# Performance work log

Measured on AMD Instinct MI355X. Metric: run time of the kernel, lower is better.

## Reference

```python
import jax, jax.numpy as jnp
import numpy as np

N_NODES = 50000
N_EDGES = 600000
D_FEAT = 128
HIDDEN = 128
OUT = 64


def sage_conv(x, src, dst, Wl, bl, Wr, n_nodes):
    # message = x[src] gathered per edge; mean-aggregated at dst
    msg = x[src]                                            # [E, d]
    agg = jax.ops.segment_sum(msg, dst, num_segments=n_nodes)   # [N, d]
    cnt = jax.ops.segment_sum(jnp.ones((src.shape[0],), x.dtype), dst,
                              num_segments=n_nodes)             # [N]
    mean = agg / jnp.maximum(cnt, 1.0)[:, None]
    # PyG SAGEConv: lin_l(mean_neighbors) + lin_r(x_root); only lin_l has bias
    return mean @ Wl + bl + x @ Wr


def setup_inputs() -> dict:
    key = jax.random.key(0)
    ks = jax.random.split(key, 7)
    x = jax.random.normal(ks[0], (N_NODES, D_FEAT), dtype=jnp.float32)
    edge_index = jax.random.randint(ks[1], (2, N_EDGES), 0, N_NODES, dtype=jnp.int64)
    s1 = 1.0 / np.sqrt(D_FEAT)
    s2 = 1.0 / np.sqrt(HIDDEN)
    W1l = jax.random.normal(ks[2], (D_FEAT, HIDDEN), dtype=jnp.float32) * s1
    b1l = jnp.zeros((HIDDEN,), dtype=jnp.float32)
    W1r = jax.random.normal(ks[3], (D_FEAT, HIDDEN), dtype=jnp.float32) * s1
    W2l = jax.random.normal(ks[4], (HIDDEN, OUT), dtype=jnp.float32) * s2
    b2l = jnp.zeros((OUT,), dtype=jnp.float32)
    W2r = jax.random.normal(ks[5], (HIDDEN, OUT), dtype=jnp.float32) * s2
    return {"x": x, "edge_index": edge_index, "W1l": W1l, "b1l": b1l,
            "W1r": W1r, "W2l": W2l, "b2l": b2l, "W2r": W2r}


def reference(x, edge_index, W1l, b1l, W1r, W2l, b2l, W2r):
    n = x.shape[0]
    src, dst = edge_index[0], edge_index[1]
    h = sage_conv(x, src, dst, W1l, b1l, W1r, n)
    h = jax.nn.relu(h)
    out = sage_conv(h, src, dst, W2l, b2l, W2r, n)
    return out
```

## Files before the change

### kernel.cpp

```cpp
#include <hip/hip_runtime.h>
#include <cstdint>
#include <cstddef>

#define D 128
#define O2 64
#define PAD 136
#define CAP 64

typedef __attribute__((ext_vector_type(8))) short bf16x8;
typedef __attribute__((ext_vector_type(4))) float f32x4;

__device__ inline unsigned short f2bf(float f) {
  union { float f; uint32_t u; } v; v.f = f;
  uint32_t r = v.u + 0x7FFF + ((v.u >> 16) & 1);
  return (unsigned short)(r >> 16);
}
__device__ inline float bf_lo(uint32_t w) {
  union { uint32_t u; float f; } v; v.u = w << 16; return v.f;
}
__device__ inline float bf_hi(uint32_t w) {
  union { uint32_t u; float f; } v; v.u = w & 0xFFFF0000u; return v.f;
}

__device__ __forceinline__ void gather16(
    const unsigned short* __restrict__ xb, const unsigned short* __restrict__ bucket,
    int cnt, int j, float a[16])
{
  int p = 0;
  for (; p + 8 <= cnt; p += 8) {
    uint4 bi = *(const uint4*)(bucket + p);
    int s[8];
    s[0] = bi.x & 0xFFFF; s[1] = bi.x >> 16;
    s[2] = bi.y & 0xFFFF; s[3] = bi.y >> 16;
    s[4] = bi.z & 0xFFFF; s[5] = bi.z >> 16;
    s[6] = bi.w & 0xFFFF; s[7] = bi.w >> 16;
    uint4 v0[8], v1[8];
    #pragma unroll
    for (int q = 0; q < 8; q++) {
      const unsigned short* r = xb + (size_t)s[q] * 128 + j * 16;
      v0[q] = *(const uint4*)r;
      v1[q] = *(const uint4*)(r + 8);
    }
    #pragma unroll
    for (int q = 0; q < 8; q++) {
      a[0]+=bf_lo(v0[q].x); a[1]+=bf_hi(v0[q].x);
      a[2]+=bf_lo(v0[q].y); a[3]+=bf_hi(v0[q].y);
      a[4]+=bf_lo(v0[q].z); a[5]+=bf_hi(v0[q].z);
      a[6]+=bf_lo(v0[q].w); a[7]+=bf_hi(v0[q].w);
      a[8]+=bf_lo(v1[q].x); a[9]+=bf_hi(v1[q].x);
      a[10]+=bf_lo(v1[q].y); a[11]+=bf_hi(v1[q].y);
      a[12]+=bf_lo(v1[q].z); a[13]+=bf_hi(v1[q].z);
      a[14]+=bf_lo(v1[q].w); a[15]+=bf_hi(v1[q].w);
    }
  }
  for (; p + 4 <= cnt; p += 4) {
    uint2 bi = *(const uint2*)(bucket + p);
    int s[4];
    s[0] = bi.x & 0xFFFF; s[1] = bi.x >> 16;
    s[2] = bi.y & 0xFFFF; s[3] = bi.y >> 16;
    uint4 v0[4], v1[4];
    #pragma unroll
    for (int q = 0; q < 4; q++) {
      const unsigned short* r = xb + (size_t)s[q] * 128 + j * 16;
      v0[q] = *(const uint4*)r;
      v1[q] = *(const uint4*)(r + 8);
    }
    #pragma unroll
    for (int q = 0; q < 4; q++) {
      a[0]+=bf_lo(v0[q].x); a[1]+=bf_hi(v0[q].x);
      a[2]+=bf_lo(v0[q].y); a[3]+=bf_hi(v0[q].y);
      a[4]+=bf_lo(v0[q].z); a[5]+=bf_hi(v0[q].z);
      a[6]+=bf_lo(v0[q].w); a[7]+=bf_hi(v0[q].w);
      a[8]+=bf_lo(v1[q].x); a[9]+=bf_hi(v1[q].x);
      a[10]+=bf_lo(v1[q].y); a[11]+=bf_hi(v1[q].y);
      a[12]+=bf_lo(v1[q].z); a[13]+=bf_hi(v1[q].z);
      a[14]+=bf_lo(v1[q].w); a[15]+=bf_hi(v1[q].w);
    }
  }
  for (; p < cnt; p++) {
    const unsigned short* rA = xb + (size_t)bucket[p] * 128 + j * 16;
    uint4 vA0 = *(const uint4*)rA, vA1 = *(const uint4*)(rA + 8);
    a[0]+=bf_lo(vA0.x); a[1]+=bf_hi(vA0.x); a[2]+=bf_lo(vA0.y); a[3]+=bf_hi(vA0.y);
    a[4]+=bf_lo(vA0.z); a[5]+=bf_hi(vA0.z); a[6]+=bf_lo(vA0.w); a[7]+=bf_hi(vA0.w);
    a[8]+=bf_lo(vA1.x); a[9]+=bf_hi(vA1.x); a[10]+=bf_lo(vA1.y); a[11]+=bf_hi(vA1.y);
    a[12]+=bf_lo(vA1.z); a[13]+=bf_hi(vA1.z); a[14]+=bf_lo(vA1.w); a[15]+=bf_hi(vA1.w);
  }
}

__global__ __launch_bounds__(256) void prep_all(
    const int* __restrict__ src, const int* __restrict__ dst,
    int* __restrict__ deg, unsigned short* __restrict__ eidx, int n_edges,
    const float* __restrict__ x, const float* __restrict__ W1l,
    const float* __restrict__ W1r, const float* __restrict__ W2l,
    const float* __restrict__ W2r, unsigned short* __restrict__ xb,
    unsigned short* __restrict__ WT1, unsigned short* __restrict__ WT2,
    int n_nodes, int edge_blocks, int xb_blocks)
{
  int b = blockIdx.x;
  if (b < edge_blocks) {
    const int half = n_edges >> 1;
    int e = b * 256 + threadIdx.x;
    if (e < half) {
      int d0 = dst[e],        d1 = dst[e + half];
      int s0 = src[e],        s1 = src[e + half];
      int p0 = atomicAdd(&deg[d0], 1);
      int p1 = atomicAdd(&deg[d1], 1);
      if (p0 < CAP)
        __builtin_nontemporal_store((unsigned short)s0, eidx + (size_t)d0 * CAP + p0);
      if (p1 < CAP)
        __builtin_nontemporal_store((unsigned short)s1, eidx + (size_t)d1 * CAP + p1);
    }
  } else if (b < edge_blocks + xb_blocks) {
    int i = (b - edge_blocks) * 256 + threadIdx.x;
    if (i < n_nodes * 32) {
      int n = i >> 5, q = i & 31;
      float4 v = ((const float4*)x)[(size_t)n * 32 + q];
      unsigned long long o =
          (unsigned long long)f2bf(v.x)
        | ((unsigned long long)f2bf(v.y) << 16)
        | ((unsigned long long)f2bf(v.z) << 32)
        | ((unsigned long long)f2bf(v.w) << 48);
      __builtin_nontemporal_store(o, (unsigned long long*)(xb + (size_t)n * 128 + q * 4));
    }
  } else {
    int t = (b - edge_blocks - xb_blocks) * 256 + threadIdx.x;
    if (t < 128 * 256) {
      int n = t >> 8, k = t & 255;
      float w = (k < 128) ? W1l[(size_t)k * 128 + n] : W1r[(size_t)(k - 128) * 128 + n];
      WT1[t] = f2bf(w);
    } else {
      int u = t - 128 * 256;
      if (u < 128 * 128) {
        int n = u >> 7, k = u & 127;
        float w = (n < 64) ? W2l[(size_t)k * 64 + n] : W2r[(size_t)k * 64 + (n - 64)];
        WT2[u] = f2bf(w);
      }
    }
  }
}

__global__ __launch_bounds__(256, 5) void fused_l12(
    const unsigned short* __restrict__ xb, const unsigned short* __restrict__ eidx,
    const int* __restrict__ deg, const unsigned short* __restrict__ WT1,
    const unsigned short* __restrict__ WT2, const float* __restrict__ b1l,
    unsigned short* __restrict__ hl, float* __restrict__ outp, int n_nodes)
{
  __shared__ unsigned short s_m[32 * PAD];
  __shared__ unsigned short s_h[32 * PAD];
  const int NB0 = blockIdx.x * 32;

  {
    const int j = threadIdx.x & 7;
    const int g = threadIdx.x >> 3;
    const int n = NB0 + g;
    float a[16];
    #pragma unroll
    for (int i = 0; i < 16; i++) a[i] = 0.f;
    float ic = 0.f;
    if (n < n_nodes) {
      const int dg = deg[n];
      const int cnt = min(dg, CAP);
      gather16(xb, eidx + (size_t)n * CAP, cnt, j, a);
      ic = 1.0f / fmaxf((float)dg, 1.0f);
    }
    uint4 o0, o1;
    o0.x = ((uint32_t)f2bf(a[1]*ic) << 16) | f2bf(a[0]*ic);
    o0.y = ((uint32_t)f2bf(a[3]*ic) << 16) | f2bf(a[2]*ic);
    o0.z = ((uint32_t)f2bf(a[5]*ic) << 16) | f2bf(a[4]*ic);
    o0.w = ((uint32_t)f2bf(a[7]*ic) << 16) | f2bf(a[6]*ic);
    o1.x = ((uint32_t)f2bf(a[9]*ic) << 16) | f2bf(a[8]*ic);
    o1.y = ((uint32_t)f2bf(a[11]*ic) << 16) | f2bf(a[10]*ic);
    o1.z = ((uint32_t)f2bf(a[13]*ic) << 16) | f2bf(a[12]*ic);
    o1.w = ((uint32_t)f2bf(a[15]*ic) << 16) | f2bf(a[14]*ic);
    unsigned short* mr = s_m + g * PAD + j * 16;
    *(uint4*)mr = o0;
    *(uint4*)(mr + 8) = o1;
  }
  __syncthreads();

  const int lane = threadIdx.x & 63;
  const int w    = threadIdx.x >> 6;
  const int rg   = w >> 1;
  const int ch   = w & 1;
  const int quad = lane >> 4, l15 = lane & 15;
  const int N0 = NB0 + rg * 16;
  const int ra = min(N0 + l15, n_nodes - 1);

  bf16x8 af[8];
  #pragma unroll
  for (int s = 0; s < 4; s++) {
    af[s]     = *(const bf16x8*)(s_m + (rg * 16 + l15) * PAD + quad * 8 + s * 32);
    af[s + 4] = *(const bf16x8*)(xb + (size_t)ra * 128 + quad * 8 + s * 32);
  }

  f32x4 acc[4];
  #pragma unroll
  for (int tt = 0; tt < 4; tt++) acc[tt] = (f32x4){0.f, 0.f, 0.f, 0.f};

  const unsigned short* b1 = WT1 + (size_t)(ch * 4) * 16 * 256 + (size_t)l15 * 256 + quad * 8;
  #pragma unroll
  for (int tt = 0; tt < 4; tt++) {
    #pragma unroll
    for (int s = 0; s < 8; s++) {
      bf16x8 bw = *(const bf16x8*)(b1 + (size_t)tt * 16 * 256 + s * 32);
      acc[tt] = __builtin_amdgcn_mfma_f32_16x16x32_bf16(af[s], bw, acc[tt], 0, 0, 0);
    }
  }

  #pragma unroll
  for (int tt = 0; tt < 4; tt++) {
    int col = (ch * 4 + tt) * 16 + l15;
    float bias = b1l[col];
    #pragma unroll
    for (int r = 0; r < 4; r++)
      s_h[(rg * 16 + quad * 4 + r) * PAD + col] = f2bf(fmaxf(acc[tt][r] + bias, 0.f));
  }
  __syncthreads();

  bf16x8 af2[4];
  #pragma unroll
  for (int s = 0; s < 4; s++)
    af2[s] = *(const bf16x8*)(s_h + (rg * 16 + l15) * PAD + quad * 8 + s * 32);

  f32x4 acc2[4];
  #pragma unroll
  for (int tt = 0; tt < 4; tt++) acc2[tt] = (f32x4){0.f, 0.f, 0.f, 0.f};

  const unsigned short* b2 = WT2 + (size_t)(ch * 4) * 16 * 128 + (size_t)l15 * 128 + quad * 8;
  #pragma unroll
  for (int tt = 0; tt < 4; tt++) {
    #pragma unroll
    for (int s = 0; s < 4; s++) {
      bf16x8 bw = *(const bf16x8*)(b2 + (size_t)tt * 16 * 128 + s * 32);
      acc2[tt] = __builtin_amdgcn_mfma_f32_16x16x32_bf16(af2[s], bw, acc2[tt], 0, 0, 0);
    }
  }

  #pragma unroll
  for (int tt = 0; tt < 4; tt++) {
    int gcol = (ch * 4 + tt) * 16 + l15;
    #pragma unroll
    for (int r = 0; r < 4; r++) {
      int row = N0 + quad * 4 + r;
      if (row < n_nodes) {
        if (ch == 0) hl[(size_t)row * 64 + gcol] = f2bf(acc2[tt][r]);
        else         outp[(size_t)row * 64 + (gcol - 64)] = acc2[tt][r];
      }
    }
  }
}

__global__ __launch_bounds__(256) void gather2_kernel(
    const unsigned short* __restrict__ hl, const unsigned short* __restrict__ eidx,
    const int* __restrict__ deg, const float* __restrict__ b2l,
    float* __restrict__ out, int n_nodes)
{
  const int j = threadIdx.x & 7;
  const int g = threadIdx.x >> 3;
  const int n = blockIdx.x * 32 + g;
  if (n >= n_nodes) return;
  const int dg = deg[n];
  const int cnt = min(dg, CAP);
  const unsigned short* bucket = eidx + (size_t)n * CAP;
  float a[8];
  #pragma unroll
  for (int i = 0; i < 8; i++) a[i] = 0.f;
  int p = 0;
  for (; p + 8 <= cnt; p += 8) {
    uint4 bi = *(const uint4*)(bucket + p);
    int s[8];
    s[0] = bi.x & 0xFFFF; s[1] = bi.x >> 16;
    s[2] = bi.y & 0xFFFF; s[3] = bi.y >> 16;
    s[4] = bi.z & 0xFFFF; s[5] = bi.z >> 16;
    s[6] = bi.w & 0xFFFF; s[7] = bi.w >> 16;
    uint4 v[8];
    #pragma unroll
    for (int q = 0; q < 8; q++)
      v[q] = *(const uint4*)(hl + (size_t)s[q] * 64 + j * 8);
    #pragma unroll
    for (int q = 0; q < 8; q++) {
      a[0]+=bf_lo(v[q].x); a[1]+=bf_hi(v[q].x);
      a[2]+=bf_lo(v[q].y); a[3]+=bf_hi(v[q].y);
      a[4]+=bf_lo(v[q].z); a[5]+=bf_hi(v[q].z);
      a[6]+=bf_lo(v[q].w); a[7]+=bf_hi(v[q].w);
    }
  }
  for (; p + 4 <= cnt; p += 4) {
    uint2 bi = *(const uint2*)(bucket + p);
    int s[4];
    s[0] = bi.x & 0xFFFF; s[1] = bi.x >> 16;
    s[2] = bi.y & 0xFFFF; s[3] = bi.y >> 16;
    uint4 v[4];
    #pragma unroll
    for (int q = 0; q < 4; q++)
      v[q] = *(const uint4*)(hl + (size_t)s[q] * 64 + j * 8);
    #pragma unroll
    for (int q = 0; q < 4; q++) {
      a[0]+=bf_lo(v[q].x); a[1]+=bf_hi(v[q].x);
      a[2]+=bf_lo(v[q].y); a[3]+=bf_hi(v[q].y);
      a[4]+=bf_lo(v[q].z); a[5]+=bf_hi(v[q].z);
      a[6]+=bf_lo(v[q].w); a[7]+=bf_hi(v[q].w);
    }
  }
  for (; p < cnt; p++) {
    uint4 vA = *(const uint4*)(hl + (size_t)bucket[p] * 64 + j * 8);
    a[0]+=bf_lo(vA.x); a[1]+=bf_hi(vA.x); a[2]+=bf_lo(vA.y); a[3]+=bf_hi(vA.y);
    a[4]+=bf_lo(vA.z); a[5]+=bf_hi(vA.z); a[6]+=bf_lo(vA.w); a[7]+=bf_hi(vA.w);
  }
  const float ic = 1.0f / fmaxf((float)dg, 1.0f);
  float* o = out + (size_t)n * 64 + j * 8;
  const float* bb = b2l + j * 8;
  float4 p0 = *(const float4*)(o);
  float4 p1 = *(const float4*)(o + 4);
  p0.x += bb[0] + a[0] * ic; p0.y += bb[1] + a[1] * ic;
  p0.z += bb[2] + a[2] * ic; p0.w += bb[3] + a[3] * ic;
  p1.x += bb[4] + a[4] * ic; p1.y += bb[5] + a[5] * ic;
  p1.z += bb[6] + a[6] * ic; p1.w += bb[7] + a[7] * ic;
  *(float4*)(o) = p0;
  *(float4*)(o + 4) = p1;
}

extern "C" void kernel_launch(void* const* d_in, const int* in_sizes, int n_in,
                              void* d_out, int out_size, void* d_ws, size_t ws_size,
                              hipStream_t stream)
{
  const float* x   = (const float*)d_in[0];
  const int*   ei  = (const int*)d_in[1];
  const float* W1l = (const float*)d_in[2];
  const float* b1l = (const float*)d_in[3];
  const float* W1r = (const float*)d_in[4];
  const float* W2l = (const float*)d_in[5];
  const float* b2l = (const float*)d_in[6];
  const float* W2r = (const float*)d_in[7];
  float* out = (float*)d_out;

  const int n_nodes = in_sizes[0] / D;
  const int n_edges = in_sizes[1] / 2;
  const int* src = ei;
  const int* dst = ei + n_edges;

  char* ws = (char*)d_ws;
  auto align256 = [](size_t v) { return (v + 255) & ~(size_t)255; };
  const size_t szN = align256((size_t)n_nodes * 4);

  size_t o = 0;
  int* deg = (int*)(ws + o);  o += szN;
  unsigned short* eidx = (unsigned short*)(ws + o); o += align256((size_t)n_nodes * CAP * 2);
  unsigned short* WT1  = (unsigned short*)(ws + o); o += align256(128 * 256 * 2);
  unsigned short* WT2  = (unsigned short*)(ws + o); o += align256(128 * 128 * 2);
  unsigned short* xb   = (unsigned short*)(ws + o); o += align256((size_t)n_nodes * 128 * 2);
  unsigned short* hl   = (unsigned short*)(ws + o); o += align256((size_t)n_nodes * 64 * 2);

  hipMemsetAsync(deg, 0, szN, stream);

  const int half = n_edges >> 1;
  const int edge_blocks = (half + 255) / 256;
  const int xb_blocks = (n_nodes * 32 + 255) / 256;
  const int w_blocks  = (128 * 256 + 128 * 128 + 255) / 256;

  prep_all<<<edge_blocks + xb_blocks + w_blocks, 256, 0, stream>>>(
      src, dst, deg, eidx, n_edges,
      x, W1l, W1r, W2l, W2r, xb, WT1, WT2, n_nodes, edge_blocks, xb_blocks);

  fused_l12<<<(n_nodes + 31) / 32, 256, 0, stream>>>(
      xb, eidx, deg, WT1, WT2, b1l, hl, out, n_nodes);

  gather2_kernel<<<(n_nodes + 31) / 32, 256, 0, stream>>>(
      hl, eidx, deg, b2l, out, n_nodes);
}
```

Before: 203.4 us.

## Restructure fused layer kernel into single-wave blocks of 16 nodes

The fused layer-1/layer-2 kernel now runs one 64-thread wavefront per 16-node block instead of four waves per 32 nodes. Each wave handles the full gather (4 lanes per node with 32 accumulators), then computes all 8 output tiles of both MFMA GEMMs, and reuses a single LDS buffer. Nontemporal stores in the prep kernel become ordinary stores. The aim is less block-level synchronisation and LDS use, in exchange for fewer lanes per node during the gather, more register pressure, and less memory-level parallelism per node.

```diff
diff --git a/kernel.cpp b/kernel.cpp
--- a/kernel.cpp
+++ b/kernel.cpp
@@ -22,69 +22,11 @@
   union { uint32_t u; float f; } v; v.u = w & 0xFFFF0000u; return v.f;
 }
 
-__device__ __forceinline__ void gather16(
-    const unsigned short* __restrict__ xb, const unsigned short* __restrict__ bucket,
-    int cnt, int j, float a[16])
-{
-  int p = 0;
-  for (; p + 8 <= cnt; p += 8) {
-    uint4 bi = *(const uint4*)(bucket + p);
-    int s[8];
-    s[0] = bi.x & 0xFFFF; s[1] = bi.x >> 16;
-    s[2] = bi.y & 0xFFFF; s[3] = bi.y >> 16;
-    s[4] = bi.z & 0xFFFF; s[5] = bi.z >> 16;
-    s[6] = bi.w & 0xFFFF; s[7] = bi.w >> 16;
-    uint4 v0[8], v1[8];
-    #pragma unroll
-    for (int q = 0; q < 8; q++) {
-      const unsigned short* r = xb + (size_t)s[q] * 128 + j * 16;
-      v0[q] = *(const uint4*)r;
-      v1[q] = *(const uint4*)(r + 8);
-    }
-    #pragma unroll
-    for (int q = 0; q < 8; q++) {
-      a[0]+=bf_lo(v0[q].x); a[1]+=bf_hi(v0[q].x);
-      a[2]+=bf_lo(v0[q].y); a[3]+=bf_hi(v0[q].y);
-      a[4]+=bf_lo(v0[q].z); a[5]+=bf_hi(v0[q].z);
-      a[6]+=bf_lo(v0[q].w); a[7]+=bf_hi(v0[q].w);
-      a[8]+=bf_lo(v1[q].x); a[9]+=bf_hi(v1[q].x);
-      a[10]+=bf_lo(v1[q].y); a[11]+=bf_hi(v1[q].y);
-      a[12]+=bf_lo(v1[q].z); a[13]+=bf_hi(v1[q].z);
-      a[14]+=bf_lo(v1[q].w); a[15]+=bf_hi(v1[q].w);
-    }
-  }
-  for (; p + 4 <= cnt; p += 4) {
-    uint2 bi = *(const uint2*)(bucket + p);
-    int s[4];
-    s[0] = bi.x & 0xFFFF; s[1] = bi.x >> 16;
-    s[2] = bi.y & 0xFFFF; s[3] = bi.y >> 16;
-    uint4 v0[4], v1[4];
-    #pragma unroll
-    for (int q = 0; q < 4; q++) {
-      const unsigned short* r = xb + (size_t)s[q] * 128 + j * 16;
-      v0[q] = *(const uint4*)r;
-      v1[q] = *(const uint4*)(r + 8);
-    }
-    #pragma unroll
-    for (int q = 0; q < 4; q++) {
-      a[0]+=bf_lo(v0[q].x); a[1]+=bf_hi(v0[q].x);
-      a[2]+=bf_lo(v0[q].y); a[3]+=bf_hi(v0[q].y);
-      a[4]+=bf_lo(v0[q].z); a[5]+=bf_hi(v0[q].z);
-      a[6]+=bf_lo(v0[q].w); a[7]+=bf_hi(v0[q].w);
-      a[8]+=bf_lo(v1[q].x); a[9]+=bf_hi(v1[q].x);
-      a[10]+=bf_lo(v1[q].y); a[11]+=bf_hi(v1[q].y);
-      a[12]+=bf_lo(v1[q].z); a[13]+=bf_hi(v1[q].z);
-      a[14]+=bf_lo(v1[q].w); a[15]+=bf_hi(v1[q].w);
-    }
-  }
-  for (; p < cnt; p++) {
-    const unsigned short* rA = xb + (size_t)bucket[p] * 128 + j * 16;
-    uint4 vA0 = *(const uint4*)rA, vA1 = *(const uint4*)(rA + 8);
-    a[0]+=bf_lo(vA0.x); a[1]+=bf_hi(vA0.x); a[2]+=bf_lo(vA0.y); a[3]+=bf_hi(vA0.y);
-    a[4]+=bf_lo(vA0.z); a[5]+=bf_hi(vA0.z); a[6]+=bf_lo(vA0.w); a[7]+=bf_hi(vA0.w);
-    a[8]+=bf_lo(vA1.x); a[9]+=bf_hi(vA1.x); a[10]+=bf_lo(vA1.y); a[11]+=bf_hi(vA1.y);
-    a[12]+=bf_lo(vA1.z); a[13]+=bf_hi(vA1.z); a[14]+=bf_lo(vA1.w); a[15]+=bf_hi(vA1.w);
-  }
+__device__ __forceinline__ void acc8(float* a, uint4 v) {
+  a[0]+=bf_lo(v.x); a[1]+=bf_hi(v.x);
+  a[2]+=bf_lo(v.y); a[3]+=bf_hi(v.y);
+  a[4]+=bf_lo(v.z); a[5]+=bf_hi(v.z);
+  a[6]+=bf_lo(v.w); a[7]+=bf_hi(v.w);
 }
 
 __global__ __launch_bounds__(256) void prep_all(
@@ -105,10 +47,8 @@
       int s0 = src[e],        s1 = src[e + half];
       int p0 = atomicAdd(&deg[d0], 1);
       int p1 = atomicAdd(&deg[d1], 1);
-      if (p0 < CAP)
-        __builtin_nontemporal_store((unsigned short)s0, eidx + (size_t)d0 * CAP + p0);
-      if (p1 < CAP)
-        __builtin_nontemporal_store((unsigned short)s1, eidx + (size_t)d1 * CAP + p1);
+      if (p0 < CAP) eidx[(size_t)d0 * CAP + p0] = (unsigned short)s0;
+      if (p1 < CAP) eidx[(size_t)d1 * CAP + p1] = (unsigned short)s1;
     }
   } else if (b < edge_blocks + xb_blocks) {
     int i = (b - edge_blocks) * 256 + threadIdx.x;
@@ -120,7 +60,7 @@
         | ((unsigned long long)f2bf(v.y) << 16)
         | ((unsigned long long)f2bf(v.z) << 32)
         | ((unsigned long long)f2bf(v.w) << 48);
-      __builtin_nontemporal_store(o, (unsigned long long*)(xb + (size_t)n * 128 + q * 4));
+      *(unsigned long long*)(xb + (size_t)n * 128 + q * 4) = o;
     }
   } else {
     int t = (b - edge_blocks - xb_blocks) * 256 + threadIdx.x;
@@ -139,96 +79,111 @@
   }
 }
 
-__global__ __launch_bounds__(256, 5) void fused_l12(
+__global__ __launch_bounds__(64) void fused_g1l12(
     const unsigned short* __restrict__ xb, const unsigned short* __restrict__ eidx,
     const int* __restrict__ deg, const unsigned short* __restrict__ WT1,
     const unsigned short* __restrict__ WT2, const float* __restrict__ b1l,
     unsigned short* __restrict__ hl, float* __restrict__ outp, int n_nodes)
 {
-  __shared__ unsigned short s_m[32 * PAD];
-  __shared__ unsigned short s_h[32 * PAD];
-  const int NB0 = blockIdx.x * 32;
-
-  {
-    const int j = threadIdx.x & 7;
-    const int g = threadIdx.x >> 3;
-    const int n = NB0 + g;
-    float a[16];
-    #pragma unroll
-    for (int i = 0; i < 16; i++) a[i] = 0.f;
-    float ic = 0.f;
-    if (n < n_nodes) {
-      const int dg = deg[n];
-      const int cnt = min(dg, CAP);
-      gather16(xb, eidx + (size_t)n * CAP, cnt, j, a);
-      ic = 1.0f / fmaxf((float)dg, 1.0f);
-    }
-    uint4 o0, o1;
-    o0.x = ((uint32_t)f2bf(a[1]*ic) << 16) | f2bf(a[0]*ic);
-    o0.y = ((uint32_t)f2bf(a[3]*ic) << 16) | f2bf(a[2]*ic);
-    o0.z = ((uint32_t)f2bf(a[5]*ic) << 16) | f2bf(a[4]*ic);
-    o0.w = ((uint32_t)f2bf(a[7]*ic) << 16) | f2bf(a[6]*ic);
-    o1.x = ((uint32_t)f2bf(a[9]*ic) << 16) | f2bf(a[8]*ic);
-    o1.y = ((uint32_t)f2bf(a[11]*ic) << 16) | f2bf(a[10]*ic);
-    o1.z = ((uint32_t)f2bf(a[13]*ic) << 16) | f2bf(a[12]*ic);
-    o1.w = ((uint32_t)f2bf(a[15]*ic) << 16) | f2bf(a[14]*ic);
-    unsigned short* mr = s_m + g * PAD + j * 16;
-    *(uint4*)mr = o0;
-    *(uint4*)(mr + 8) = o1;
+  __shared__ unsigned short sx[16 * PAD];
+  const int lane = threadIdx.x;
+  const int g = lane >> 2;
+  const int c = lane & 3;
+  const int c8 = c * 8;
+  const int N0 = blockIdx.x * 16;
+  const int n = N0 + g;
+
+  float a[32];
+  #pragma unroll
+  for (int i = 0; i < 32; i++) a[i] = 0.f;
+  int dg = 0;
+  if (n < n_nodes) dg = deg[n];
+  const int cnt = min(dg, CAP);
+  const unsigned short* bucket = eidx + (size_t)n * CAP;
+  int p = 0;
+  for (; p + 4 <= cnt; p += 4) {
+    uint2 bi = *(const uint2*)(bucket + p);
+    int s0 = bi.x & 0xFFFF, s1 = bi.x >> 16;
+    int s2 = bi.y & 0xFFFF, s3 = bi.y >> 16;
+    const unsigned short* r0 = xb + (size_t)s0 * 128 + c8;
+    const unsigned short* r1 = xb + (size_t)s1 * 128 + c8;
+    const unsigned short* r2 = xb + (size_t)s2 * 128 + c8;
+    const unsigned short* r3 = xb + (size_t)s3 * 128 + c8;
+    uint4 v[16];
+    #pragma unroll
+    for (int k = 0; k < 4; k++) {
+      v[k]      = *(const uint4*)(r0 + k * 32);
+      v[4 + k]  = *(const uint4*)(r1 + k * 32);
+      v[8 + k]  = *(const uint4*)(r2 + k * 32);
+      v[12 + k] = *(const uint4*)(r3 + k * 32);
+    }
+    #pragma unroll
+    for (int q = 0; q < 4; q++)
+      #pragma unroll
+      for (int k = 0; k < 4; k++)
+        acc8(&a[k * 8], v[q * 4 + k]);
+  }
+  for (; p < cnt; p++) {
+    const unsigned short* r = xb + (size_t)bucket[p] * 128 + c8;
+    #pragma unroll
+    for (int k = 0; k < 4; k++) acc8(&a[k * 8], *(const uint4*)(r + k * 32));
+  }
+
+  const float ic = (n < n_nodes) ? 1.0f / fmaxf((float)dg, 1.0f) : 0.f;
+  #pragma unroll
+  for (int k = 0; k < 4; k++) {
+    uint4 o;
+    o.x = ((uint32_t)f2bf(a[k*8+1]*ic) << 16) | f2bf(a[k*8+0]*ic);
+    o.y = ((uint32_t)f2bf(a[k*8+3]*ic) << 16) | f2bf(a[k*8+2]*ic);
+    o.z = ((uint32_t)f2bf(a[k*8+5]*ic) << 16) | f2bf(a[k*8+4]*ic);
+    o.w = ((uint32_t)f2bf(a[k*8+7]*ic) << 16) | f2bf(a[k*8+6]*ic);
+    *(uint4*)(sx + g * PAD + k * 32 + c8) = o;
   }
   __syncthreads();
 
-  const int lane = threadIdx.x & 63;
-  const int w    = threadIdx.x >> 6;
-  const int rg   = w >> 1;
-  const int ch   = w & 1;
   const int quad = lane >> 4, l15 = lane & 15;
-  const int N0 = NB0 + rg * 16;
   const int ra = min(N0 + l15, n_nodes - 1);
 
   bf16x8 af[8];
   #pragma unroll
   for (int s = 0; s < 4; s++) {
-    af[s]     = *(const bf16x8*)(s_m + (rg * 16 + l15) * PAD + quad * 8 + s * 32);
+    af[s]     = *(const bf16x8*)(sx + l15 * PAD + quad * 8 + s * 32);
     af[s + 4] = *(const bf16x8*)(xb + (size_t)ra * 128 + quad * 8 + s * 32);
   }
-
-  f32x4 acc[4];
-  #pragma unroll
-  for (int tt = 0; tt < 4; tt++) acc[tt] = (f32x4){0.f, 0.f, 0.f, 0.f};
-
-  const unsigned short* b1 = WT1 + (size_t)(ch * 4) * 16 * 256 + (size_t)l15 * 256 + quad * 8;
-  #pragma unroll
-  for (int tt = 0; tt < 4; tt++) {
+  f32x4 acc[8];
+  #pragma unroll
+  for (int tt = 0; tt < 8; tt++) acc[tt] = (f32x4){0.f, 0.f, 0.f, 0.f};
+  const unsigned short* b1 = WT1 + (size_t)l15 * 256 + quad * 8;
+  #pragma unroll
+  for (int tt = 0; tt < 8; tt++) {
     #pragma unroll
     for (int s = 0; s < 8; s++) {
       bf16x8 bw = *(const bf16x8*)(b1 + (size_t)tt * 16 * 256 + s * 32);
       acc[tt] = __builtin_amdgcn_mfma_f32_16x16x32_bf16(af[s], bw, acc[tt], 0, 0, 0);
     }
   }
-
-  #pragma unroll
-  for (int tt = 0; tt < 4; tt++) {
-    int col = (ch * 4 + tt) * 16 + l15;
+  __syncthreads();
+
+  #pragma unroll
+  for (int tt = 0; tt < 8; tt++) {
+    int col = tt * 16 + l15;
     float bias = b1l[col];
     #pragma unroll
     for (int r = 0; r < 4; r++)
-      s_h[(rg * 16 + quad * 4 + r) * PAD + col] = f2bf(fmaxf(acc[tt][r] + bias, 0.f));
+      sx[(quad * 4 + r) * PAD + col] = f2bf(fmaxf(acc[tt][r] + bias, 0.f));
   }
   __syncthreads();
 
   bf16x8 af2[4];
   #pragma unroll
   for (int s = 0; s < 4; s++)
-    af2[s] = *(const bf16x8*)(s_h + (rg * 16 + l15) * PAD + quad * 8 + s * 32);
-
-  f32x4 acc2[4];
-  #pragma unroll
-  for (int tt = 0; tt < 4; tt++) acc2[tt] = (f32x4){0.f, 0.f, 0.f, 0.f};
-
-  const unsigned short* b2 = WT2 + (size_t)(ch * 4) * 16 * 128 + (size_t)l15 * 128 + quad * 8;
-  #pragma unroll
-  for (int tt = 0; tt < 4; tt++) {
+    af2[s] = *(const bf16x8*)(sx + l15 * PAD + quad * 8 + s * 32);
+  f32x4 acc2[8];
+  #pragma unroll
+  for (int tt = 0; tt < 8; tt++) acc2[tt] = (f32x4){0.f, 0.f, 0.f, 0.f};
+  const unsigned short* b2 = WT2 + (size_t)l15 * 128 + quad * 8;
+  #pragma unroll
+  for (int tt = 0; tt < 8; tt++) {
     #pragma unroll
     for (int s = 0; s < 4; s++) {
       bf16x8 bw = *(const bf16x8*)(b2 + (size_t)tt * 16 * 128 + s * 32);
@@ -237,14 +192,14 @@
   }
 
   #pragma unroll
-  for (int tt = 0; tt < 4; tt++) {
-    int gcol = (ch * 4 + tt) * 16 + l15;
+  for (int tt = 0; tt < 8; tt++) {
+    int col = tt * 16 + l15;
     #pragma unroll
     for (int r = 0; r < 4; r++) {
       int row = N0 + quad * 4 + r;
       if (row < n_nodes) {
-        if (ch == 0) hl[(size_t)row * 64 + gcol] = f2bf(acc2[tt][r]);
-        else         outp[(size_t)row * 64 + (gcol - 64)] = acc2[tt][r];
+        if (tt < 4) hl[(size_t)row * 64 + col] = f2bf(acc2[tt][r]);
+        else        outp[(size_t)row * 64 + (col - 64)] = acc2[tt][r];
       }
     }
   }
@@ -278,12 +233,7 @@
     for (int q = 0; q < 8; q++)
       v[q] = *(const uint4*)(hl + (size_t)s[q] * 64 + j * 8);
     #pragma unroll
-    for (int q = 0; q < 8; q++) {
-      a[0]+=bf_lo(v[q].x); a[1]+=bf_hi(v[q].x);
-      a[2]+=bf_lo(v[q].y); a[3]+=bf_hi(v[q].y);
-      a[4]+=bf_lo(v[q].z); a[5]+=bf_hi(v[q].z);
-      a[6]+=bf_lo(v[q].w); a[7]+=bf_hi(v[q].w);
-    }
+    for (int q = 0; q < 8; q++) acc8(a, v[q]);
   }
   for (; p + 4 <= cnt; p += 4) {
     uint2 bi = *(const uint2*)(bucket + p);
@@ -295,17 +245,11 @@
     for (int q = 0; q < 4; q++)
       v[q] = *(const uint4*)(hl + (size_t)s[q] * 64 + j * 8);
     #pragma unroll
-    for (int q = 0; q < 4; q++) {
-      a[0]+=bf_lo(v[q].x); a[1]+=bf_hi(v[q].x);
-      a[2]+=bf_lo(v[q].y); a[3]+=bf_hi(v[q].y);
-      a[4]+=bf_lo(v[q].z); a[5]+=bf_hi(v[q].z);
-      a[6]+=bf_lo(v[q].w); a[7]+=bf_hi(v[q].w);
-    }
+    for (int q = 0; q < 4; q++) acc8(a, v[q]);
   }
   for (; p < cnt; p++) {
     uint4 vA = *(const uint4*)(hl + (size_t)bucket[p] * 64 + j * 8);
-    a[0]+=bf_lo(vA.x); a[1]+=bf_hi(vA.x); a[2]+=bf_lo(vA.y); a[3]+=bf_hi(vA.y);
-    a[4]+=bf_lo(vA.z); a[5]+=bf_hi(vA.z); a[6]+=bf_lo(vA.w); a[7]+=bf_hi(vA.w);
+    acc8(a, vA);
   }
   const float ic = 1.0f / fmaxf((float)dg, 1.0f);
   float* o = out + (size_t)n * 64 + j * 8;
@@ -362,7 +306,7 @@
       src, dst, deg, eidx, n_edges,
       x, W1l, W1r, W2l, W2r, xb, WT1, WT2, n_nodes, edge_blocks, xb_blocks);
 
-  fused_l12<<<(n_nodes + 31) / 32, 256, 0, stream>>>(
+  fused_g1l12<<<(n_nodes + 15) / 16, 64, 0, stream>>>(
       xb, eidx, deg, WT1, WT2, b1l, hl, out, n_nodes);
 
   gather2_kernel<<<(n_nodes + 31) / 32, 256, 0, stream>>>(
```

After: 196.8 us. 1.03x faster.
